# Optimization experiments

Measured on AMD Instinct MI355X. Metric: run time of the kernel, lower is better.

Reference implementation:

```python
import jax, jax.numpy as jnp
import numpy as np

B, T, N, D, FF, E, L, K = 4, 12, 2000, 16, 64, 4, 2, 2
EA, H = 3000, 3
BETA, CW = 0.01, 0.001


def setup_inputs() -> dict:
    key = jax.random.key(0)
    ks = iter(jax.random.split(key, 40))
    nrm = lambda shape, s=0.02: jax.random.normal(next(ks), shape, jnp.float32) * s
    inp = {}
    inp['x'] = jax.random.normal(next(ks), (B, T, N), jnp.float32)
    inp['velo'] = jax.random.uniform(next(ks), (B, T, N), jnp.float32)
    inp['adj_haversine'] = jax.random.uniform(next(ks), (N, N), jnp.float32) + 0.05
    inp['laplacian_diff'] = jax.random.normal(next(ks), (N, N), jnp.float32)
    inp['laplacian_heat'] = jax.random.normal(next(ks), (N, N), jnp.float32)
    inp['start_w'] = nrm((1, D)); inp['start_b'] = jnp.zeros((D,), jnp.float32)
    inp['gate_w'] = nrm((L, D, E))
    inp['exp_w1'] = nrm((L, E, D, FF)); inp['exp_b1'] = jnp.zeros((L, E, FF), jnp.float32)
    inp['exp_w2'] = nrm((L, E, FF, D)); inp['exp_b2'] = jnp.zeros((L, E, D), jnp.float32)
    inp['proj_w'] = nrm((T * D, T)); inp['proj_b'] = jnp.zeros((T,), jnp.float32)
    inp['lt_w'] = nrm((N, EA)); inp['lt_b'] = jnp.zeros((EA,), jnp.float32)
    inp['qkv_w'] = nrm((EA, 3 * EA)); inp['qkv_b'] = jnp.zeros((3 * EA,), jnp.float32)
    inp['attn_out_w'] = nrm((EA, EA)); inp['attn_out_b'] = jnp.zeros((EA,), jnp.float32)
    inp['ll_w'] = nrm((EA, N)); inp['ll_b'] = jnp.zeros((N,), jnp.float32)
    inp['p2_w'] = nrm((T, T)); inp['p2_b'] = jnp.zeros((T,), jnp.float32)
    return inp


def reference(x, velo, adj_haversine, laplacian_diff, laplacian_heat, start_w, start_b,
              gate_w, exp_w1, exp_b1, exp_w2, exp_b2, proj_w, proj_b, lt_w, lt_b,
              qkv_w, qkv_b, attn_out_w, attn_out_b, ll_w, ll_b, p2_w, p2_b):
    # start_fc: [B,T,N,1] -> [B,T,N,D]
    out = x[..., None] @ start_w + start_b
    balance = jnp.float32(0.0)
    cv = lambda v: v.var() / (v.mean() ** 2 + 1e-10)
    for l in range(L):  # AMS mixture-of-experts stack (noisy top-k gating, eval mode)
        feat = out.mean(axis=(1, 2))                      # [B,D]
        logits = feat @ gate_w[l]                          # [B,E]
        topv, topi = jax.lax.top_k(logits, K)
        g = jax.nn.softmax(topv, axis=-1)
        gates = jnp.zeros((B, E), out.dtype).at[jnp.arange(B)[:, None], topi].set(g)
        h = jax.nn.gelu(jnp.einsum('btnd,edf->ebtnf', out, exp_w1[l]) + exp_b1[l][:, None, None, None, :])
        y = jnp.einsum('ebtnf,efd->ebtnd', h, exp_w2[l]) + exp_b2[l][:, None, None, None, :]
        out = out + jnp.einsum('be,ebtnd->btnd', gates, y)  # residual_connection
        imp = gates.sum(0)
        load = (gates > 0).astype(out.dtype).sum(0)
        balance = balance + cv(imp) + cv(load)
    # wavelet layer: 1-level smoothing split along time
    low = lambda z: 0.5 * (z + jnp.roll(z, 1, axis=1))
    low_T = low(x)
    high_V = velo - low(velo)
    # navier-stokes-style graph laplacian from velocities
    v0 = velo[0, 0]                                        # [N]
    G = jnp.maximum(0.0, v0[:, None] / adj_haversine)
    G = jnp.where(jnp.isinf(G), 0.0, G)
    lap_ns = jnp.diag(G.sum(1)) - G
    std = lambda m: (m - m.mean()) / m.std()
    lap_d = std(laplacian_diff); lap_h = std(laplacian_heat)
    lap_ns = jnp.nan_to_num(std(lap_ns))
    # trunk projection: [B,T,N,D] -> [B,T,N]
    outp = (out.transpose(0, 2, 1, 3).reshape(B, N, T * D) @ proj_w + proj_b).transpose(0, 2, 1)
    # laplacian-fused matmuls
    r1 = low_T @ lap_d; r2 = high_V @ lap_ns; r3 = low_T @ lap_h
    rng01 = lambda m: (m - m.min()) / jnp.maximum(m.max() - m.min(), 1e-8)
    lin = lambda m: (rng01(m) @ lt_w + lt_b).transpose(1, 0, 2)   # [T,B,EA]
    r1, r2, r3 = lin(r1), lin(r2), lin(r3)
    hd = EA // H
    wq, wk, wv = jnp.split(qkv_w, 3, axis=1)
    bq, bk, bv = jnp.split(qkv_b, 3)
    def mha(q, k, v):
        qh = (q @ wq + bq).reshape(T, B, H, hd)
        kh = (k @ wk + bk).reshape(T, B, H, hd)
        vh = (v @ wv + bv).reshape(T, B, H, hd)
        sc = jnp.einsum('sbhd,tbhd->bhst', qh, kh) * (1.0 / np.sqrt(hd))
        a = jax.nn.softmax(sc, axis=-1)
        o = jnp.einsum('bhst,tbhd->sbhd', a, vh).reshape(T, B, EA)
        return o @ attn_out_w + attn_out_b
    o1 = mha(r1, r2, r3); o2 = mha(r2, r3, r1); o3 = mha(r3, r1, r2)
    back = lambda o: (o @ ll_w + ll_b).transpose(1, 0, 2)         # [B,T,N]
    out2 = BETA * (back(o1) + back(o2) + back(o3))
    out2 = (out2.reshape(-1, T) @ p2_w + p2_b).reshape(B, N, T).transpose(0, 2, 1)
    out_3 = outp + out2
    # contrastive loss between trunk and laplacian branch
    f1 = outp.transpose(0, 2, 1).reshape(B * N, T)
    f2 = out2.transpose(0, 2, 1).reshape(B * N, T)
    nz = lambda f: f / jnp.maximum(jnp.linalg.norm(f, axis=1, keepdims=True), 1e-12)
    sim = (nz(f1) @ nz(f2).T) / 0.1                               # [8000, 8000]
    closs = -jnp.mean(jnp.diagonal(jax.nn.log_softmax(sim, axis=1)))
    return out_3, balance, CW * closs
```

## Files before the change

kernel.cpp:

```cpp
#include <hip/hip_runtime.h>
#include <math.h>

namespace {
constexpr int B_ = 4, T_ = 12, N_ = 2000, D_ = 16, FF_ = 64, E_ = 4, L_ = 2;
constexpr int EA_ = 3000, H_ = 3, HD_ = EA_ / H_;
constexpr int BT_ = B_ * T_;
constexpr int R3_ = 3 * BT_;
constexpr long long NN_ = (long long)N_ * N_;
constexpr int BTN_ = B_ * T_ * N_;
constexpr float BETA_ = 0.01f, CW_ = 0.001f;
constexpr int RKS_ = 20;
constexpr int RKC_ = 100;
constexpr int KP3 = 3008;
constexpr int KP2 = 2016;

constexpr size_t OFF_OUT4 = 0;
constexpr size_t OFF_LOWT = OFF_OUT4 + (size_t)BTN_ * D_;
constexpr size_t OFF_HVT  = OFF_LOWT + BTN_;
constexpr size_t OFF_ALIN = OFF_HVT + BTN_;
constexpr size_t OFF_RT   = OFF_ALIN + (size_t)N_ * R3_;
constexpr size_t OFF_P    = OFF_RT + (size_t)EA_ * R3_;
constexpr size_t OFF_AOT  = OFF_P + (size_t)R3_ * 3 * EA_;
constexpr size_t OFF_OT   = OFF_AOT + (size_t)EA_ * R3_;
constexpr size_t OFF_O2P  = OFF_OT + (size_t)EA_ * R3_;
constexpr size_t OFF_OUTP = OFF_O2P + BTN_;
constexpr size_t OFF_O2F  = OFF_OUTP + BTN_;
constexpr size_t OFF_LI   = OFF_O2F + BTN_;
constexpr size_t OFF_S    = OFF_LI + 8000;
constexpr size_t OFF_RSL  = OFF_S + 2000;
constexpr size_t OFF_RSH  = OFF_RSL + 48;
constexpr size_t OFF_STP  = OFF_RSH + 48;
constexpr size_t OFF_STAT = OFF_STP + 3072;
constexpr size_t OFF_MMP  = OFF_STAT + 8;
constexpr size_t OFF_AB   = OFF_MMP + 384;
constexpr size_t OFF_CSP  = OFF_AB + 8;
constexpr size_t OFF_CS   = OFF_CSP + 48000;
constexpr size_t OFF_FEAT = OFF_CS + 3000;
constexpr size_t OFF_GATE = OFF_FEAT + 64;
constexpr size_t OFF_BAL  = OFF_GATE + 16;
constexpr size_t OFF_PART = ((OFF_BAL + 1 + 255) & ~(size_t)255);
constexpr size_t PARTCAP  = 13000000;
constexpr size_t OFF_AT_LIN= OFF_PART + PARTCAP;
constexpr size_t OFF_AT_Q  = OFF_AT_LIN + (size_t)R3_ * KP2 / 2;
constexpr size_t OFF_AT_AO = OFF_AT_Q + (size_t)R3_ * KP3 / 2;
constexpr size_t OFF_AT_LL = OFF_AT_AO + (size_t)R3_ * KP3 / 2;
constexpr size_t OFF_G1B   = OFF_AT_LL + (size_t)R3_ * KP3 / 2;
constexpr size_t OFF_G2B   = OFF_G1B + 128000;
}

typedef __attribute__((ext_vector_type(8))) short short8;
typedef __attribute__((ext_vector_type(4))) float f32x4;

__device__ __forceinline__ float waveReduceSum(float v) {
  for (int off = 32; off; off >>= 1) v += __shfl_down(v, off);
  return v;
}

__device__ __forceinline__ unsigned short f2bf(float x) {
  unsigned int u = __float_as_uint(x);
  unsigned int r = (u + 0x7FFFu + ((u >> 16) & 1u)) >> 16;
  return (unsigned short)r;
}

__device__ __forceinline__ size_t aidx(int row, int k) {
  return ((size_t)(k >> 3) * R3_ + row) * 8 + (k & 7);
}

__device__ __forceinline__ void fma16(float* __restrict__ acc,
                                      const float4* __restrict__ a4, float bv) {
#pragma unroll
  for (int r4 = 0; r4 < 4; ++r4) {
    float4 av = a4[r4];
    acc[r4 * 4 + 0] = fmaf(av.x, bv, acc[r4 * 4 + 0]);
    acc[r4 * 4 + 1] = fmaf(av.y, bv, acc[r4 * 4 + 1]);
    acc[r4 * 4 + 2] = fmaf(av.z, bv, acc[r4 * 4 + 2]);
    acc[r4 * 4 + 3] = fmaf(av.w, bv, acc[r4 * 4 + 3]);
  }
}

__global__ void k_init(float* ws) {
  if (threadIdx.x == 0) ws[OFF_BAL] = 0.f;
}

__global__ void k_start(const float* __restrict__ x, const float* __restrict__ sw,
                        const float* __restrict__ sb, float* __restrict__ out4) {
  int i = blockIdx.x * 256 + threadIdx.x;
  if (i >= BTN_ * D_) return;
  int d = i & 15;
  out4[i] = fmaf(x[i >> 4], sw[d], sb[d]);
}

__global__ void k_feat(const float* __restrict__ out4, float* __restrict__ feat) {
  int b = blockIdx.x >> 4, d = blockIdx.x & 15;
  float s = 0.f;
  for (int tn = threadIdx.x; tn < T_ * N_; tn += 256)
    s += out4[((size_t)b * T_ * N_ + tn) * D_ + d];
  __shared__ float red[4];
  s = waveReduceSum(s);
  if ((threadIdx.x & 63) == 0) red[threadIdx.x >> 6] = s;
  __syncthreads();
  if (threadIdx.x == 0)
    feat[blockIdx.x] = (red[0] + red[1] + red[2] + red[3]) * (1.f / (T_ * N_));
}

__global__ void k_gate(const float* __restrict__ feat, const float* __restrict__ gw,
                       float* __restrict__ ws, int l) {
  __shared__ float lg[B_ * E_];
  int tid = threadIdx.x;
  if (tid < B_ * E_) {
    int b = tid >> 2, e = tid & 3;
    float s = 0.f;
    for (int d = 0; d < D_; ++d) s = fmaf(feat[b * D_ + d], gw[(l * D_ + d) * E_ + e], s);
    lg[tid] = s;
  }
  __syncthreads();
  if (tid == 0) {
    float* gates = ws + OFF_GATE;
    float imp[E_] = {0, 0, 0, 0}, load[E_] = {0, 0, 0, 0};
    for (int i = 0; i < B_ * E_; ++i) gates[i] = 0.f;
    for (int b = 0; b < B_; ++b) {
      const float* lb = lg + b * E_;
      int i1 = 0; float v1 = lb[0];
      for (int e = 1; e < E_; ++e) if (lb[e] > v1) { v1 = lb[e]; i1 = e; }
      int i2 = -1; float v2 = -1e30f;
      for (int e = 0; e < E_; ++e) { if (e == i1) continue; if (lb[e] > v2) { v2 = lb[e]; i2 = e; } }
      float e2 = expf(v2 - v1);
      float den = 1.f + e2;
      float g1 = 1.f / den, g2 = e2 / den;
      gates[b * E_ + i1] = g1; gates[b * E_ + i2] = g2;
      imp[i1] += g1; imp[i2] += g2; load[i1] += 1.f; load[i2] += 1.f;
    }
    float bal = 0.f;
    float m = 0.f; for (int e = 0; e < E_; ++e) m += imp[e]; m *= 0.25f;
    float v = 0.f; for (int e = 0; e < E_; ++e) { float d = imp[e] - m; v += d * d; } v *= 0.25f;
    bal += v / (m * m + 1e-10f);
    m = 0.f; for (int e = 0; e < E_; ++e) m += load[e]; m *= 0.25f;
    v = 0.f; for (int e = 0; e < E_; ++e) { float d = load[e] - m; v += d * d; } v *= 0.25f;
    bal += v / (m * m + 1e-10f);
    ws[OFF_BAL] += bal;
  }
}

__global__ void k_expert(float* __restrict__ out4, const float* __restrict__ w1,
                         const float* __restrict__ b1, const float* __restrict__ w2,
                         const float* __restrict__ b2, const float* __restrict__ ws, int l) {
  int b = blockIdx.y;
  int tn = blockIdx.x * 256 + threadIdx.x;
  if (tn >= T_ * N_) return;
  float* row = out4 + ((size_t)b * T_ * N_ + tn) * D_;
  float r[D_], acc[D_];
#pragma unroll
  for (int d = 0; d < D_; ++d) { r[d] = row[d]; acc[d] = r[d]; }
  const float* gates = ws + OFF_GATE;
  for (int e = 0; e < E_; ++e) {
    float g = gates[b * E_ + e];
    if (g <= 0.f) continue;
    const float* W1 = w1 + (size_t)(l * E_ + e) * D_ * FF_;
    const float* B1 = b1 + (size_t)(l * E_ + e) * FF_;
    const float* W2 = w2 + (size_t)(l * E_ + e) * FF_ * D_;
    const float* B2 = b2 + (size_t)(l * E_ + e) * D_;
#pragma unroll 4
    for (int f = 0; f < FF_; ++f) {
      float p = B1[f];
#pragma unroll
      for (int d = 0; d < D_; ++d) p = fmaf(r[d], W1[d * FF_ + f], p);
      float c2 = 1.5957691216057308f * (p + 0.044715f * p * p * p);
      float e1 = __expf(-c2);
      float hv = p * __builtin_amdgcn_rcpf(1.f + e1);
      float gh = g * hv;
#pragma unroll
      for (int d = 0; d < D_; ++d) acc[d] = fmaf(gh, W2[f * D_ + d], acc[d]);
    }
#pragma unroll
    for (int d = 0; d < D_; ++d) acc[d] = fmaf(g, B2[d], acc[d]);
  }
#pragma unroll
  for (int d = 0; d < D_; ++d) row[d] = acc[d];
}

__global__ void k_wavelet(const float* __restrict__ x, const float* __restrict__ velo,
                          float* __restrict__ lowT, float* __restrict__ hvT) {
  int i = blockIdx.x * 256 + threadIdx.x;
  if (i >= BTN_) return;
  int b = i / (T_ * N_);
  int t = (i / N_) % T_;
  int n = i % N_;
  int ip = b * T_ * N_ + ((t + T_ - 1) % T_) * N_ + n;
  int row = t * B_ + b;
  lowT[(size_t)n * BT_ + row] = 0.5f * (x[i] + x[ip]);
  hvT[(size_t)n * BT_ + row] = 0.5f * (velo[i] - velo[ip]);
}

__global__ void k_rowsum(const float* __restrict__ lowT, const float* __restrict__ hvT,
                         float* __restrict__ ws) {
  int which = blockIdx.x / BT_;
  int row = blockIdx.x % BT_;
  const float* M = which ? hvT : lowT;
  float s = 0.f;
  for (int n = threadIdx.x; n < N_; n += 256) s += M[(size_t)n * BT_ + row];
  __shared__ float red[4];
  s = waveReduceSum(s);
  if ((threadIdx.x & 63) == 0) red[threadIdx.x >> 6] = s;
  __syncthreads();
  if (threadIdx.x == 0) ws[(which ? OFF_RSH : OFF_RSL) + row] = red[0] + red[1] + red[2] + red[3];
}

__global__ void k_S(const float* __restrict__ adj, const float* __restrict__ v0,
                    float* __restrict__ S) {
  int m = blockIdx.x;
  float vm = v0[m];
  const float* a = adj + (size_t)m * N_;
  float s = 0.f;
  for (int n = threadIdx.x; n < N_; n += 256) s += vm / a[n];
  __shared__ float red[4];
  s = waveReduceSum(s);
  if ((threadIdx.x & 63) == 0) red[threadIdx.x >> 6] = s;
  __syncthreads();
  if (threadIdx.x == 0) S[m] = red[0] + red[1] + red[2] + red[3];
}

__global__ void k_stats3(const float* __restrict__ lapd, const float* __restrict__ laph,
                         const float* __restrict__ adj, const float* __restrict__ v0,
                         const float* __restrict__ S, float* __restrict__ stp) {
  int z = blockIdx.z;
  float s = 0.f, ss = 0.f;
  if (z < 2) {
    const float* M = z ? laph : lapd;
    for (long long i = blockIdx.x * 256 + threadIdx.x; i < NN_; i += 512 * 256) {
      float v = M[i];
      s += v; ss = fmaf(v, v, ss);
    }
  } else {
    for (long long i = blockIdx.x * 256 + threadIdx.x; i < NN_; i += 512 * 256) {
      int m = (int)(i / N_), n = (int)(i % N_);
      float e = -(v0[m] / adj[i]);
      if (m == n) e += S[m];
      s += e; ss = fmaf(e, e, ss);
    }
  }
  __shared__ float r1[4], r2[4];
  for (int off = 32; off; off >>= 1) { s += __shfl_down(s, off); ss += __shfl_down(ss, off); }
  if ((threadIdx.x & 63) == 0) { r1[threadIdx.x >> 6] = s; r2[threadIdx.x >> 6] = ss; }
  __syncthreads();
  if (threadIdx.x == 0) {
    float* p = stp + (size_t)z * 1024;
    p[blockIdx.x * 2] = r1[0] + r1[1] + r1[2] + r1[3];
    p[blockIdx.x * 2 + 1] = r2[0] + r2[1] + r2[2] + r2[3];
  }
}

__global__ void k_stats2(const float* __restrict__ stp, float* __restrict__ stat) {
  int z = blockIdx.x;
  const float* part = stp + (size_t)z * 1024;
  float s = 0.f, ss = 0.f;
  for (int i = threadIdx.x; i < 512; i += 256) { s += part[i * 2]; ss += part[i * 2 + 1]; }
  __shared__ float r1[4], r2[4];
  for (int off = 32; off; off >>= 1) { s += __shfl_down(s, off); ss += __shfl_down(ss, off); }
  if ((threadIdx.x & 63) == 0) { r1[threadIdx.x >> 6] = s; r2[threadIdx.x >> 6] = ss; }
  __syncthreads();
  if (threadIdx.x == 0) {
    float su = r1[0] + r1[1] + r1[2] + r1[3];
    float sq = r2[0] + r2[1] + r2[2] + r2[3];
    float mu = su * (1.f / (float)NN_);
    float var = sq * (1.f / (float)NN_) - mu * mu;
    stat[2 * z] = mu;
    stat[2 * z + 1] = 1.f / sqrtf(var);
  }
}

__global__ __launch_bounds__(256) void k_rgemm3(
    const float* __restrict__ lowT, const float* __restrict__ hvT,
    const float* __restrict__ lapd, const float* __restrict__ laph,
    const float* __restrict__ adj, const float* __restrict__ v0,
    const float* __restrict__ S, float* __restrict__ part) {
  int zz = blockIdx.z;
  int z = zz / 3, rg = zz % 3;
  int col = blockIdx.x * 256 + threadIdx.x;
  int m0 = blockIdx.y * RKC_;
  int m1 = min(N_, m0 + RKC_);
  float acc[16];
#pragma unroll
  for (int r = 0; r < 16; ++r) acc[r] = 0.f;
  if (col < N_) {
    const float* Abase = (z == 1 ? hvT : lowT);
    const float* ap = Abase + (size_t)m0 * BT_ + rg * 16;
    if (z != 1) {
      const float* Bm = z ? laph : lapd;
      const float* bp = Bm + (size_t)m0 * N_ + col;
      int len = m1 - m0;
      int ng = len >> 3;
      float bc[8];
      if (ng > 0) {
#pragma unroll
        for (int u = 0; u < 8; ++u) bc[u] = bp[(size_t)u * N_];
      }
      for (int gi = 0; gi < ng; ++gi) {
        float bn[8];
        bool more = (gi + 1 < ng);
        if (more) {
#pragma unroll
          for (int u = 0; u < 8; ++u) bn[u] = bp[(size_t)(8 + u) * N_];
        }
#pragma unroll
        for (int u = 0; u < 8; ++u)
          fma16(acc, (const float4*)(ap + (size_t)u * BT_), bc[u]);
        ap += (size_t)8 * BT_;
        bp += (size_t)8 * N_;
        if (more) {
#pragma unroll
          for (int u = 0; u < 8; ++u) bc[u] = bn[u];
        }
      }
      for (int m = m0 + (ng << 3); m < m1; ++m) {
        fma16(acc, (const float4*)ap, *bp);
        ap += BT_;
        bp += N_;
      }
    } else {
      const float* jp = adj + (size_t)m0 * N_ + col;
      int len = m1 - m0;
      int ng = len >> 3;
      float jc[8];
      if (ng > 0) {
#pragma unroll
        for (int u = 0; u < 8; ++u) jc[u] = jp[(size_t)u * N_];
      }
      int m = m0;
      for (int gi = 0; gi < ng; ++gi) {
        float jn[8];
        bool more = (gi + 1 < ng);
        if (more) {
#pragma unroll
          for (int u = 0; u < 8; ++u) jn[u] = jp[(size_t)(8 + u) * N_];
        }
#pragma unroll
        for (int u = 0; u < 8; ++u) {
          float bv = -(v0[m + u] / jc[u]);
          if (m + u == col) bv += S[m + u];
          fma16(acc, (const float4*)(ap + (size_t)u * BT_), bv);
        }
        m += 8;
        ap += (size_t)8 * BT_;
        jp += (size_t)8 * N_;
        if (more) {
#pragma unroll
          for (int u = 0; u < 8; ++u) jc[u] = jn[u];
        }
      }
      for (; m < m1; ++m) {
        float bv = -(v0[m] / (*jp));
        if (m == col) bv += S[m];
        fma16(acc, (const float4*)ap, bv);
        ap += BT_;
        jp += N_;
      }
    }
    float* pp = part + (((size_t)z * RKS_ + blockIdx.y) * BT_ + rg * 16) * N_ + col;
#pragma unroll
    for (int r = 0; r < 16; ++r) pp[(size_t)r * N_] = acc[r];
  }
}

__global__ void k_epiR3(const float* __restrict__ part, float* __restrict__ ws,
                        unsigned short* __restrict__ atl) {
  int z = blockIdx.z;
  int n = blockIdx.x * 256 + threadIdx.x;
  int row = blockIdx.y;
  if (n >= KP2) return;
  int arow = z * BT_ + row;
  if (n >= N_) { atl[aidx(arow, n)] = 0; return; }
  const float* base = part + (size_t)z * RKS_ * BT_ * N_;
  float s = 0.f;
  for (int ks = 0; ks < RKS_; ++ks) s += base[((size_t)(ks * BT_ + row)) * N_ + n];
  int statIdx = (z == 0) ? 0 : (z == 1 ? 4 : 2);
  size_t rsOff = (z == 1) ? OFF_RSH : OFF_RSL;
  float mu = ws[OFF_STAT + statIdx], isd = ws[OFF_STAT + statIdx + 1];
  float val = (s - mu * ws[rsOff + row]) * isd;
  ws[OFF_ALIN + (size_t)n * R3_ + arow] = val;
  atl[aidx(arow, n)] = f2bf(val);
}

__global__ __launch_bounds__(256) void k_mfmaW(
    const unsigned short* __restrict__ At, const float* __restrict__ W,
    float* __restrict__ part, int Nc, int Kp, int K, int stepChunk) {
  __shared__ unsigned int lds[2][128][21];
  int tid = threadIdx.x;
  int lane = tid & 63, w = tid >> 6;
  int lr = lane & 15, lo = lane >> 4;
  int colBase = blockIdx.x * 128;
  int stepsTot = Kp / 32;
  int s0 = blockIdx.y * stepChunk;
  int s1 = min(stepsTot, s0 + stepChunk);
  int cg = tid & 31, kr8 = tid >> 5;
  int c0l = 4 * cg;
  bool fullC = (colBase + 128 <= Nc);

  f32x4 acc[18];
#pragma unroll
  for (int mt = 0; mt < 18; ++mt) {
    acc[mt][0] = 0.f; acc[mt][1] = 0.f; acc[mt][2] = 0.f; acc[mt][3] = 0.f;
  }

  auto stage = [&](int s, int buf) {
#pragma unroll
    for (int h = 0; h < 2; ++h) {
      int kp = kr8 + 8 * h;
      int kA = s * 32 + 2 * kp;
      int kB = kA + 1;
      float4 r0 = {0.f, 0.f, 0.f, 0.f}, r1 = {0.f, 0.f, 0.f, 0.f};
      int c0 = colBase + c0l;
      if (fullC) {
        if (kA < K) r0 = *(const float4*)(W + (size_t)kA * Nc + c0);
        if (kB < K) r1 = *(const float4*)(W + (size_t)kB * Nc + c0);
      } else {
        float rr0[4] = {0.f, 0.f, 0.f, 0.f}, rr1[4] = {0.f, 0.f, 0.f, 0.f};
#pragma unroll
        for (int e = 0; e < 4; ++e) {
          if (c0 + e < Nc) {
            if (kA < K) rr0[e] = W[(size_t)kA * Nc + c0 + e];
            if (kB < K) rr1[e] = W[(size_t)kB * Nc + c0 + e];
          }
        }
        r0.x = rr0[0]; r0.y = rr0[1]; r0.z = rr0[2]; r0.w = rr0[3];
        r1.x = rr1[0]; r1.y = rr1[1]; r1.z = rr1[2]; r1.w = rr1[3];
      }
      lds[buf][c0l + 0][kp] = ((unsigned int)f2bf(r1.x) << 16) | f2bf(r0.x);
      lds[buf][c0l + 1][kp] = ((unsigned int)f2bf(r1.y) << 16) | f2bf(r0.y);
      lds[buf][c0l + 2][kp] = ((unsigned int)f2bf(r1.z) << 16) | f2bf(r0.z);
      lds[buf][c0l + 3][kp] = ((unsigned int)f2bf(r1.w) << 16) | f2bf(r0.w);
    }
  };

  if (s0 < s1) stage(s0, 0);
  __syncthreads();

  const unsigned short* ap = At + ((size_t)(s0 * 4 + lo) * R3_ + lr) * 8;
  const size_t apStep = (size_t)4 * R3_ * 8;
  int lcol0 = w * 32 + lr;
  int lcol1 = w * 32 + 16 + lr;
  for (int s = s0; s < s1; ++s) {
    int buf = (s - s0) & 1;
    union { unsigned int u[4]; short8 s8; } b0, b1;
#pragma unroll
    for (int j = 0; j < 4; ++j) {
      b0.u[j] = lds[buf][lcol0][lo * 4 + j];
      b1.u[j] = lds[buf][lcol1][lo * 4 + j];
    }
#pragma unroll
    for (int mt = 0; mt < 9; ++mt) {
      short8 a = *(const short8*)(ap + (size_t)mt * 128);
      acc[mt] = __builtin_amdgcn_mfma_f32_16x16x32_bf16(a, b0.s8, acc[mt], 0, 0, 0);
      acc[9 + mt] = __builtin_amdgcn_mfma_f32_16x16x32_bf16(a, b1.s8, acc[9 + mt], 0, 0, 0);
    }
    if (s + 1 < s1) stage(s + 1, buf ^ 1);
    __syncthreads();
    ap += apStep;
  }

#pragma unroll
  for (int half = 0; half < 2; ++half) {
    int gcol = colBase + w * 32 + half * 16 + lr;
    if (gcol < Nc) {
#pragma unroll
      for (int mt = 0; mt < 9; ++mt) {
        int row = mt * 16 + lo * 4;
        float* pp = part + ((size_t)blockIdx.y * R3_ + row) * Nc + gcol;
        f32x4 a = acc[half * 9 + mt];
        pp[0] = a[0];
        pp[(size_t)Nc] = a[1];
        pp[2 * (size_t)Nc] = a[2];
        pp[3 * (size_t)Nc] = a[3];
      }
    }
  }
}

__global__ void k_minmax(const float* __restrict__ alin, float* __restrict__ mmp) {
  int g = blockIdx.y;
  float mn = 3.4e38f, mx = -3.4e38f;
  for (int i = blockIdx.x * 256 + threadIdx.x; i < N_ * BT_; i += 64 * 256) {
    int n = i / BT_, r = i % BT_;
    float v = alin[(size_t)n * R3_ + g * BT_ + r];
    mn = fminf(mn, v); mx = fmaxf(mx, v);
  }
  __shared__ float rn[4], rx[4];
  for (int off = 32; off; off >>= 1) {
    mn = fminf(mn, __shfl_down(mn, off));
    mx = fmaxf(mx, __shfl_down(mx, off));
  }
  if ((threadIdx.x & 63) == 0) { rn[threadIdx.x >> 6] = mn; rx[threadIdx.x >> 6] = mx; }
  __syncthreads();
  if (threadIdx.x == 0) {
    mn = fminf(fminf(rn[0], rn[1]), fminf(rn[2], rn[3]));
    mx = fmaxf(fmaxf(rx[0], rx[1]), fmaxf(rx[2], rx[3]));
    mmp[(size_t)(g * 64 + blockIdx.x) * 2] = mn;
    mmp[(size_t)(g * 64 + blockIdx.x) * 2 + 1] = mx;
  }
}

__global__ void k_minmax2(float* __restrict__ ws) {
  int g = blockIdx.x;
  int i = threadIdx.x;
  float mn = ws[OFF_MMP + (size_t)(g * 64 + i) * 2];
  float mx = ws[OFF_MMP + (size_t)(g * 64 + i) * 2 + 1];
  for (int off = 32; off; off >>= 1) {
    mn = fminf(mn, __shfl_down(mn, off));
    mx = fmaxf(mx, __shfl_down(mx, off));
  }
  if (i == 0) {
    float denom = fmaxf(mx - mn, 1e-8f);
    float a = 1.f / denom;
    ws[OFF_AB + g * 2] = a;
    ws[OFF_AB + g * 2 + 1] = -mn * a;
  }
}

__global__ void k_colsum(const float* __restrict__ ltw, float* __restrict__ csp) {
  int e = blockIdx.x * 256 + threadIdx.x;
  int ks = blockIdx.y;
  if (e >= EA_) return;
  float s = 0.f;
  for (int n = ks * 125; n < (ks + 1) * 125; ++n) s += ltw[(size_t)n * EA_ + e];
  csp[(size_t)ks * EA_ + e] = s;
}
__global__ void k_colsum2(float* __restrict__ ws) {
  int e = blockIdx.x * 256 + threadIdx.x;
  if (e >= EA_) return;
  float s = 0.f;
  for (int ks = 0; ks < 16; ++ks) s += ws[OFF_CSP + (size_t)ks * EA_ + e];
  ws[OFF_CS + e] = s;
}

__global__ void k_epiLin(const float* __restrict__ part, const float* __restrict__ ltb,
                         float* __restrict__ ws, unsigned short* __restrict__ atq,
                         int ksplit) {
  int e = blockIdx.x * 256 + threadIdx.x;
  int row = blockIdx.y;
  if (e >= KP3) return;
  if (e >= EA_) { atq[aidx(row, e)] = 0; return; }
  float s = 0.f;
  for (int ks = 0; ks < ksplit; ++ks) s += part[((size_t)(ks * R3_ + row)) * EA_ + e];
  int g = row / BT_;
  float a = ws[OFF_AB + g * 2], bb = ws[OFF_AB + g * 2 + 1];
  float val = fmaf(a, s, fmaf(bb, ws[OFF_CS + e], ltb[e]));
  atq[aidx(row, e)] = f2bf(val);
}

__global__ void k_epiQkv(const float* __restrict__ part, const float* __restrict__ qkvb,
                         float* __restrict__ P, int ksplit) {
  int c = blockIdx.x * 256 + threadIdx.x;
  int row = blockIdx.y;
  if (c >= 3 * EA_) return;
  float s = 0.f;
  for (int ks = 0; ks < ksplit; ++ks) s += part[((size_t)(ks * R3_ + row)) * (3 * EA_) + c];
  P[(size_t)row * (3 * EA_) + c] = s + qkvb[c];
}

__global__ void k_attn(const float* __restrict__ P, unsigned short* __restrict__ atao) {
  int mha = blockIdx.y;
  int s_ = blockIdx.x / (B_ * H_);
  int rem = blockIdx.x % (B_ * H_);
  int b = rem / H_, h = rem % H_;
  const int pq[3] = {0, 1, 2}, pk[3] = {1, 2, 0}, pv[3] = {2, 0, 1};
  const float* qrow = P + ((size_t)(pq[mha] * BT_ + s_ * B_ + b)) * (3 * EA_) + h * HD_;
  __shared__ float sc[T_];
  int w = threadIdx.x >> 6, lane = threadIdx.x & 63;
  for (int t = w; t < T_; t += 4) {
    const float* krow = P + ((size_t)(pk[mha] * BT_ + t * B_ + b)) * (3 * EA_) + EA_ + h * HD_;
    float p = 0.f;
    for (int d = lane; d < HD_; d += 64) p = fmaf(qrow[d], krow[d], p);
    p = waveReduceSum(p);
    if (lane == 0) sc[t] = p * 0.031622776601683794f;
  }
  __syncthreads();
  float a[T_];
  float m = sc[0];
#pragma unroll
  for (int t = 1; t < T_; ++t) m = fmaxf(m, sc[t]);
  float sum = 0.f;
#pragma unroll
  for (int t = 0; t < T_; ++t) { a[t] = expf(sc[t] - m); sum += a[t]; }
  float inv = 1.f / sum;
#pragma unroll
  for (int t = 0; t < T_; ++t) a[t] *= inv;
  int orow = mha * BT_ + s_ * B_ + b;
  for (int d = threadIdx.x; d < HD_; d += 256) {
    float o = 0.f;
#pragma unroll
    for (int t = 0; t < T_; ++t)
      o = fmaf(a[t], P[((size_t)(pv[mha] * BT_ + t * B_ + b)) * (3 * EA_) + 2 * EA_ + h * HD_ + d], o);
    atao[aidx(orow, h * HD_ + d)] = f2bf(o);
  }
  if (h == 0 && threadIdx.x < 8) atao[aidx(orow, EA_ + threadIdx.x)] = 0;
}

__global__ void k_epiAO(const float* __restrict__ part, const float* __restrict__ aob,
                        unsigned short* __restrict__ atll, int ksplit) {
  int c = blockIdx.x * 256 + threadIdx.x;
  int row = blockIdx.y;
  if (c >= KP3) return;
  if (c >= EA_) { atll[aidx(row, c)] = 0; return; }
  float s = 0.f;
  for (int ks = 0; ks < ksplit; ++ks) s += part[((size_t)(ks * R3_ + row)) * EA_ + c];
  atll[aidx(row, c)] = f2bf(s + aob[c]);
}

__global__ void k_epiLL(const float* __restrict__ part, const float* __restrict__ llb,
                        float* __restrict__ o2p, int ksplit) {
  int n = blockIdx.x * 256 + threadIdx.x;
  int row = blockIdx.y;
  if (n >= N_) return;
  float s = 0.f;
  for (int g = 0; g < 3; ++g)
    for (int ks = 0; ks < ksplit; ++ks)
      s += part[((size_t)(ks * R3_ + g * BT_ + row)) * N_ + n];
  int t = row / B_, b = row % B_;
  o2p[(size_t)b * (T_ * N_) + t * N_ + n] = BETA_ * (s + 3.f * llb[n]);
}

__global__ void k_proj(const float* __restrict__ out4, const float* __restrict__ pw,
                       const float* __restrict__ pb, float* __restrict__ outp) {
  int i = blockIdx.x * 256 + threadIdx.x;
  if (i >= BTN_) return;
  int b = i / (T_ * N_);
  int t = (i / N_) % T_;
  int n = i % N_;
  float acc = pb[t];
  for (int t2 = 0; t2 < T_; ++t2) {
    const float* o = out4 + ((size_t)(b * T_ + t2) * N_ + n) * D_;
#pragma unroll
    for (int d = 0; d < D_; ++d) acc = fmaf(o[d], pw[(t2 * D_ + d) * T_ + t], acc);
  }
  outp[i] = acc;
}

__global__ void k_p2(const float* __restrict__ o2p, const float* __restrict__ p2w,
                     const float* __restrict__ p2b, float* __restrict__ o2f) {
  int i = blockIdx.x * 256 + threadIdx.x;
  if (i >= BTN_) return;
  int b = i / (T_ * N_);
  int t = (i / N_) % T_;
  int n = i % N_;
  float acc = p2b[t];
  const float* src = o2p + (size_t)b * (T_ * N_) + (size_t)n * T_;
#pragma unroll
  for (int c = 0; c < T_; ++c) acc = fmaf(src[c], p2w[c * T_ + t], acc);
  o2f[i] = acc;
}

__global__ void k_fng(const float* __restrict__ outp, const float* __restrict__ o2f,
                      float* __restrict__ dout, unsigned short* __restrict__ g1b,
                      unsigned short* __restrict__ g2b) {
  int r = blockIdx.x * 256 + threadIdx.x;
  if (r >= B_ * N_) return;
  int b = r / N_, n = r % N_;
  float v1[T_], v2[T_];
  float s1 = 0.f, s2 = 0.f;
#pragma unroll
  for (int t = 0; t < T_; ++t) {
    size_t idx = (size_t)b * T_ * N_ + (size_t)t * N_ + n;
    v1[t] = outp[idx];
    v2[t] = o2f[idx];
    dout[idx] = v1[t] + v2[t];
    s1 = fmaf(v1[t], v1[t], s1);
    s2 = fmaf(v2[t], v2[t], s2);
  }
  float n1 = fmaxf(sqrtf(s1), 1e-12f), n2 = fmaxf(sqrtf(s2), 1e-12f);
  float i1 = 10.f / n1, i2 = 1.f / n2;
  unsigned short q[32], z[32];
#pragma unroll
  for (int t = 0; t < T_; ++t) { q[t] = f2bf(v1[t] * i1); z[t] = f2bf(v2[t] * i2); }
#pragma unroll
  for (int t = T_; t < 32; ++t) { q[t] = 0; z[t] = 0; }
  short8* qd = (short8*)(g1b + (size_t)r * 32);
  short8* zd = (short8*)(g2b + (size_t)r * 32);
#pragma unroll
  for (int c = 0; c < 4; ++c) {
    short8 pv, pz;
#pragma unroll
    for (int e = 0; e < 8; ++e) { pv[e] = (short)q[c * 8 + e]; pz[e] = (short)z[c * 8 + e]; }
    qd[c] = pv;
    zd[c] = pz;
  }
}

__global__ __launch_bounds__(256) void k_lsemf(const unsigned short* __restrict__ g1b,
                                               const unsigned short* __restrict__ g2b,
                                               float* __restrict__ psm,
                                               float* __restrict__ psd) {
  int lane = threadIdx.x & 63, w = threadIdx.x >> 6;
  int lr = lane & 15, lo = lane >> 4;
  int i0 = blockIdx.x * 16;
  int slice = blockIdx.y * 4 + w;
  short8 a = *(const short8*)(g1b + (size_t)(i0 + lr) * 32 + lo * 8);
  float sm[4] = {0.f, 0.f, 0.f, 0.f};
  float sd[4] = {0.f, 0.f, 0.f, 0.f};
  for (int t = slice; t < 500; t += 16) {
    int j0 = t * 16;
    short8 b = *(const short8*)(g2b + (size_t)(j0 + lr) * 32 + lo * 8);
    f32x4 acc = {0.f, 0.f, 0.f, 0.f};
    acc = __builtin_amdgcn_mfma_f32_16x16x32_bf16(a, b, acc, 0, 0, 0);
#pragma unroll
    for (int rg = 0; rg < 4; ++rg) {
      float s = acc[rg];
      sm[rg] += __expf(s);
      if (j0 + lr == i0 + lo * 4 + rg) sd[rg] = s;
    }
  }
#pragma unroll
  for (int off = 1; off < 16; off <<= 1) {
#pragma unroll
    for (int rg = 0; rg < 4; ++rg) {
      sm[rg] += __shfl_xor(sm[rg], off);
      sd[rg] += __shfl_xor(sd[rg], off);
    }
  }
  __shared__ float lsm[4][16], lsd[4][16];
  if (lr == 0) {
#pragma unroll
    for (int rg = 0; rg < 4; ++rg) {
      lsm[w][lo * 4 + rg] = sm[rg];
      lsd[w][lo * 4 + rg] = sd[rg];
    }
  }
  __syncthreads();
  if (threadIdx.x < 16) {
    float m = lsm[0][threadIdx.x] + lsm[1][threadIdx.x] + lsm[2][threadIdx.x] + lsm[3][threadIdx.x];
    float d = lsd[0][threadIdx.x] + lsd[1][threadIdx.x] + lsd[2][threadIdx.x] + lsd[3][threadIdx.x];
    psm[(size_t)blockIdx.y * 8000 + i0 + threadIdx.x] = m;
    psd[(size_t)blockIdx.y * 8000 + i0 + threadIdx.x] = d;
  }
}

__global__ __launch_bounds__(1024) void k_lsefin(const float* __restrict__ psm,
                                                 const float* __restrict__ psd,
                                                 const float* __restrict__ ws,
                                                 float* __restrict__ dout) {
  float acc = 0.f;
  for (int r = threadIdx.x; r < B_ * N_; r += 1024) {
    float sm = psm[r] + psm[8000 + r] + psm[16000 + r] + psm[24000 + r];
    float sd = psd[r] + psd[8000 + r] + psd[16000 + r] + psd[24000 + r];
    acc += sd - logf(sm);
  }
  __shared__ float red[16];
  acc = waveReduceSum(acc);
  if ((threadIdx.x & 63) == 0) red[threadIdx.x >> 6] = acc;
  __syncthreads();
  if (threadIdx.x == 0) {
    float s = 0.f;
    for (int i = 0; i < 16; ++i) s += red[i];
    float closs = -s * (1.f / (B_ * N_));
    dout[BTN_] = ws[OFF_BAL];
    dout[BTN_ + 1] = CW_ * closs;
  }
}

extern "C" void kernel_launch(void* const* d_in, const int* in_sizes, int n_in,
                              void* d_out, int out_size, void* d_ws, size_t ws_size,
                              hipStream_t stream) {
  const float* x    = (const float*)d_in[0];
  const float* velo = (const float*)d_in[1];
  const float* adj  = (const float*)d_in[2];
  const float* lapd = (const float*)d_in[3];
  const float* laph = (const float*)d_in[4];
  const float* sw   = (const float*)d_in[5];
  const float* sb   = (const float*)d_in[6];
  const float* gw   = (const float*)d_in[7];
  const float* ew1  = (const float*)d_in[8];
  const float* eb1  = (const float*)d_in[9];
  const float* ew2  = (const float*)d_in[10];
  const float* eb2  = (const float*)d_in[11];
  const float* pw   = (const float*)d_in[12];
  const float* pb   = (const float*)d_in[13];
  const float* ltw  = (const float*)d_in[14];
  const float* ltb  = (const float*)d_in[15];
  const float* qkvw = (const float*)d_in[16];
  const float* qkvb = (const float*)d_in[17];
  const float* aow  = (const float*)d_in[18];
  const float* aob  = (const float*)d_in[19];
  const float* llw  = (const float*)d_in[20];
  const float* llb  = (const float*)d_in[21];
  const float* p2w  = (const float*)d_in[22];
  const float* p2b  = (const float*)d_in[23];
  float* ws = (float*)d_ws;
  float* dout = (float*)d_out;
  const float* v0 = velo;
  float* part = ws + OFF_PART;
  unsigned short* atLin = (unsigned short*)(ws + OFF_AT_LIN);
  unsigned short* atQ   = (unsigned short*)(ws + OFF_AT_Q);
  unsigned short* atAO  = (unsigned short*)(ws + OFF_AT_AO);
  unsigned short* atLL  = (unsigned short*)(ws + OFF_AT_LL);
  unsigned short* g1b   = (unsigned short*)(ws + OFF_G1B);
  unsigned short* g2b   = (unsigned short*)(ws + OFF_G2B);
  dim3 b256(256);

  k_init<<<dim3(1), dim3(64), 0, stream>>>(ws);

  k_start<<<dim3((BTN_ * D_ + 255) / 256), b256, 0, stream>>>(x, sw, sb, ws + OFF_OUT4);

  for (int l = 0; l < L_; ++l) {
    k_feat<<<dim3(B_ * D_), b256, 0, stream>>>(ws + OFF_OUT4, ws + OFF_FEAT);
    k_gate<<<dim3(1), dim3(64), 0, stream>>>(ws + OFF_FEAT, gw, ws, l);
    k_expert<<<dim3((T_ * N_ + 255) / 256, B_), b256, 0, stream>>>(ws + OFF_OUT4, ew1, eb1, ew2, eb2, ws, l);
  }

  k_wavelet<<<dim3((BTN_ + 255) / 256), b256, 0, stream>>>(x, velo, ws + OFF_LOWT, ws + OFF_HVT);
  k_rowsum<<<dim3(2 * BT_), b256, 0, stream>>>(ws + OFF_LOWT, ws + OFF_HVT, ws);
  k_S<<<dim3(N_), b256, 0, stream>>>(adj, v0, ws + OFF_S);

  k_stats3<<<dim3(512, 1, 3), b256, 0, stream>>>(lapd, laph, adj, v0, ws + OFF_S, ws + OFF_STP);
  k_stats2<<<dim3(3), b256, 0, stream>>>(ws + OFF_STP, ws + OFF_STAT);

  k_rgemm3<<<dim3(8, RKS_, 9), b256, 0, stream>>>(ws + OFF_LOWT, ws + OFF_HVT, lapd, laph,
                                                  adj, v0, ws + OFF_S, part);
  k_epiR3<<<dim3(8, 48, 3), b256, 0, stream>>>(part, ws, atLin);

  k_minmax<<<dim3(64, 3), b256, 0, stream>>>(ws + OFF_ALIN, ws + OFF_MMP);
  k_minmax2<<<dim3(3), dim3(64), 0, stream>>>(ws);
  k_colsum<<<dim3(12, 16), b256, 0, stream>>>(ltw, ws + OFF_CSP);
  k_colsum2<<<dim3(12), b256, 0, stream>>>(ws);

  k_mfmaW<<<dim3(24, 21), b256, 0, stream>>>(atLin, ltw, part, EA_, KP2, N_, 3);
  k_epiLin<<<dim3(12, 144), b256, 0, stream>>>(part, ltb, ws, atQ, 21);

  k_mfmaW<<<dim3(71, 10), b256, 0, stream>>>(atQ, qkvw, part, 3 * EA_, KP3, EA_, 10);
  k_epiQkv<<<dim3(36, 144), b256, 0, stream>>>(part, qkvb, ws + OFF_P, 10);

  k_attn<<<dim3(T_ * B_ * H_, 3), b256, 0, stream>>>(ws + OFF_P, atAO);

  k_mfmaW<<<dim3(24, 24), b256, 0, stream>>>(atAO, aow, part, EA_, KP3, EA_, 4);
  k_epiAO<<<dim3(12, 144), b256, 0, stream>>>(part, aob, atLL, 24);

  k_mfmaW<<<dim3(16, 24), b256, 0, stream>>>(atLL, llw, part, N_, KP3, EA_, 4);
  k_epiLL<<<dim3(8, 48), b256, 0, stream>>>(part, llb, ws + OFF_O2P, 24);

  k_proj<<<dim3((BTN_ + 255) / 256), b256, 0, stream>>>(ws + OFF_OUT4, pw, pb, ws + OFF_OUTP);
  k_p2<<<dim3((BTN_ + 255) / 256), b256, 0, stream>>>(ws + OFF_O2P, p2w, p2b, ws + OFF_O2F);

  k_fng<<<dim3((B_ * N_ + 255) / 256), b256, 0, stream>>>(ws + OFF_OUTP, ws + OFF_O2F, dout, g1b, g2b);

  k_lsemf<<<dim3(500, 4), b256, 0, stream>>>(g1b, g2b, part, part + 32000);
  k_lsefin<<<dim3(1), dim3(1024), 0, stream>>>(part, part + 32000, ws, dout);
}
```

Before: 524.0 us.

## Fuse matrix mean/variance stats into rgemm3 and retune split-K counts

Removes the separate k_stats3 pass, which reread three 2000x2000 matrices (lapd, laph, and the adj-derived matrix), and instead accumulates sum and sum-of-squares inside k_rgemm3 while those matrices are already being streamed. Only blocks with rg==0 accumulate, and k_stats2 now reduces 160 partials instead of 512. It also changes the split-K chunk counts of several k_mfmaW GEMMs and their epilogues. The stats work adds a small amount of arithmetic to the GEMM inner loop, and stats2 must now run after rgemm3.

```diff
diff --git a/kernel.cpp b/kernel.cpp
--- a/kernel.cpp
+++ b/kernel.cpp
@@ -219,41 +219,11 @@
   if (threadIdx.x == 0) S[m] = red[0] + red[1] + red[2] + red[3];
 }
 
-__global__ void k_stats3(const float* __restrict__ lapd, const float* __restrict__ laph,
-                         const float* __restrict__ adj, const float* __restrict__ v0,
-                         const float* __restrict__ S, float* __restrict__ stp) {
-  int z = blockIdx.z;
-  float s = 0.f, ss = 0.f;
-  if (z < 2) {
-    const float* M = z ? laph : lapd;
-    for (long long i = blockIdx.x * 256 + threadIdx.x; i < NN_; i += 512 * 256) {
-      float v = M[i];
-      s += v; ss = fmaf(v, v, ss);
-    }
-  } else {
-    for (long long i = blockIdx.x * 256 + threadIdx.x; i < NN_; i += 512 * 256) {
-      int m = (int)(i / N_), n = (int)(i % N_);
-      float e = -(v0[m] / adj[i]);
-      if (m == n) e += S[m];
-      s += e; ss = fmaf(e, e, ss);
-    }
-  }
-  __shared__ float r1[4], r2[4];
-  for (int off = 32; off; off >>= 1) { s += __shfl_down(s, off); ss += __shfl_down(ss, off); }
-  if ((threadIdx.x & 63) == 0) { r1[threadIdx.x >> 6] = s; r2[threadIdx.x >> 6] = ss; }
-  __syncthreads();
-  if (threadIdx.x == 0) {
-    float* p = stp + (size_t)z * 1024;
-    p[blockIdx.x * 2] = r1[0] + r1[1] + r1[2] + r1[3];
-    p[blockIdx.x * 2 + 1] = r2[0] + r2[1] + r2[2] + r2[3];
-  }
-}
-
 __global__ void k_stats2(const float* __restrict__ stp, float* __restrict__ stat) {
   int z = blockIdx.x;
   const float* part = stp + (size_t)z * 1024;
   float s = 0.f, ss = 0.f;
-  for (int i = threadIdx.x; i < 512; i += 256) { s += part[i * 2]; ss += part[i * 2 + 1]; }
+  for (int i = threadIdx.x; i < 160; i += 256) { s += part[i * 2]; ss += part[i * 2 + 1]; }
   __shared__ float r1[4], r2[4];
   for (int off = 32; off; off >>= 1) { s += __shfl_down(s, off); ss += __shfl_down(ss, off); }
   if ((threadIdx.x & 63) == 0) { r1[threadIdx.x >> 6] = s; r2[threadIdx.x >> 6] = ss; }
@@ -272,12 +242,15 @@
     const float* __restrict__ lowT, const float* __restrict__ hvT,
     const float* __restrict__ lapd, const float* __restrict__ laph,
     const float* __restrict__ adj, const float* __restrict__ v0,
-    const float* __restrict__ S, float* __restrict__ part) {
+    const float* __restrict__ S, float* __restrict__ part,
+    float* __restrict__ stp) {
   int zz = blockIdx.z;
   int z = zz / 3, rg = zz % 3;
   int col = blockIdx.x * 256 + threadIdx.x;
   int m0 = blockIdx.y * RKC_;
   int m1 = min(N_, m0 + RKC_);
+  bool doStats = (rg == 0);
+  float sAcc = 0.f, ssAcc = 0.f;
   float acc[16];
 #pragma unroll
   for (int r = 0; r < 16; ++r) acc[r] = 0.f;
@@ -302,8 +275,10 @@
           for (int u = 0; u < 8; ++u) bn[u] = bp[(size_t)(8 + u) * N_];
         }
 #pragma unroll
-        for (int u = 0; u < 8; ++u)
+        for (int u = 0; u < 8; ++u) {
           fma16(acc, (const float4*)(ap + (size_t)u * BT_), bc[u]);
+          if (doStats) { sAcc += bc[u]; ssAcc = fmaf(bc[u], bc[u], ssAcc); }
+        }
         ap += (size_t)8 * BT_;
         bp += (size_t)8 * N_;
         if (more) {
@@ -312,7 +287,9 @@
         }
       }
       for (int m = m0 + (ng << 3); m < m1; ++m) {
-        fma16(acc, (const float4*)ap, *bp);
+        float bv = *bp;
+        fma16(acc, (const float4*)ap, bv);
+        if (doStats) { sAcc += bv; ssAcc = fmaf(bv, bv, ssAcc); }
         ap += BT_;
         bp += N_;
       }
@@ -338,6 +315,7 @@
           float bv = -(v0[m + u] / jc[u]);
           if (m + u == col) bv += S[m + u];
           fma16(acc, (const float4*)(ap + (size_t)u * BT_), bv);
+          if (doStats) { sAcc += bv; ssAcc = fmaf(bv, bv, ssAcc); }
         }
         m += 8;
         ap += (size_t)8 * BT_;
@@ -351,6 +329,7 @@
         float bv = -(v0[m] / (*jp));
         if (m == col) bv += S[m];
         fma16(acc, (const float4*)ap, bv);
+        if (doStats) { sAcc += bv; ssAcc = fmaf(bv, bv, ssAcc); }
         ap += BT_;
         jp += N_;
       }
@@ -358,6 +337,18 @@
     float* pp = part + (((size_t)z * RKS_ + blockIdx.y) * BT_ + rg * 16) * N_ + col;
 #pragma unroll
     for (int r = 0; r < 16; ++r) pp[(size_t)r * N_] = acc[r];
+  }
+  if (doStats) {
+    __shared__ float r1[4], r2[4];
+    float s = sAcc, ss = ssAcc;
+    for (int off = 32; off; off >>= 1) { s += __shfl_down(s, off); ss += __shfl_down(ss, off); }
+    if ((threadIdx.x & 63) == 0) { r1[threadIdx.x >> 6] = s; r2[threadIdx.x >> 6] = ss; }
+    __syncthreads();
+    if (threadIdx.x == 0) {
+      float* p = stp + (size_t)z * 1024 + ((size_t)blockIdx.y * 8 + blockIdx.x) * 2;
+      p[0] = r1[0] + r1[1] + r1[2] + r1[3];
+      p[1] = r2[0] + r2[1] + r2[2] + r2[3];
+    }
   }
 }
 
@@ -808,11 +799,9 @@
   k_rowsum<<<dim3(2 * BT_), b256, 0, stream>>>(ws + OFF_LOWT, ws + OFF_HVT, ws);
   k_S<<<dim3(N_), b256, 0, stream>>>(adj, v0, ws + OFF_S);
 
-  k_stats3<<<dim3(512, 1, 3), b256, 0, stream>>>(lapd, laph, adj, v0, ws + OFF_S, ws + OFF_STP);
+  k_rgemm3<<<dim3(8, RKS_, 9), b256, 0, stream>>>(ws + OFF_LOWT, ws + OFF_HVT, lapd, laph,
+                                                  adj, v0, ws + OFF_S, part, ws + OFF_STP);
   k_stats2<<<dim3(3), b256, 0, stream>>>(ws + OFF_STP, ws + OFF_STAT);
-
-  k_rgemm3<<<dim3(8, RKS_, 9), b256, 0, stream>>>(ws + OFF_LOWT, ws + OFF_HVT, lapd, laph,
-                                                  adj, v0, ws + OFF_S, part);
   k_epiR3<<<dim3(8, 48, 3), b256, 0, stream>>>(part, ws, atLin);
 
   k_minmax<<<dim3(64, 3), b256, 0, stream>>>(ws + OFF_ALIN, ws + OFF_MMP);
@@ -820,19 +809,19 @@
   k_colsum<<<dim3(12, 16), b256, 0, stream>>>(ltw, ws + OFF_CSP);
   k_colsum2<<<dim3(12), b256, 0, stream>>>(ws);
 
-  k_mfmaW<<<dim3(24, 21), b256, 0, stream>>>(atLin, ltw, part, EA_, KP2, N_, 3);
-  k_epiLin<<<dim3(12, 144), b256, 0, stream>>>(part, ltb, ws, atQ, 21);
+  k_mfmaW<<<dim3(24, 16), b256, 0, stream>>>(atLin, ltw, part, EA_, KP2, N_, 4);
+  k_epiLin<<<dim3(12, 144), b256, 0, stream>>>(part, ltb, ws, atQ, 16);
 
   k_mfmaW<<<dim3(71, 10), b256, 0, stream>>>(atQ, qkvw, part, 3 * EA_, KP3, EA_, 10);
   k_epiQkv<<<dim3(36, 144), b256, 0, stream>>>(part, qkvb, ws + OFF_P, 10);
 
   k_attn<<<dim3(T_ * B_ * H_, 3), b256, 0, stream>>>(ws + OFF_P, atAO);
 
-  k_mfmaW<<<dim3(24, 24), b256, 0, stream>>>(atAO, aow, part, EA_, KP3, EA_, 4);
-  k_epiAO<<<dim3(12, 144), b256, 0, stream>>>(part, aob, atLL, 24);
-
-  k_mfmaW<<<dim3(16, 24), b256, 0, stream>>>(atLL, llw, part, N_, KP3, EA_, 4);
-  k_epiLL<<<dim3(8, 48), b256, 0, stream>>>(part, llb, ws + OFF_O2P, 24);
+  k_mfmaW<<<dim3(24, 16), b256, 0, stream>>>(atAO, aow, part, EA_, KP3, EA_, 6);
+  k_epiAO<<<dim3(12, 144), b256, 0, stream>>>(part, aob, atLL, 16);
+
+  k_mfmaW<<<dim3(16, 20), b256, 0, stream>>>(atLL, llw, part, N_, KP3, EA_, 5);
+  k_epiLL<<<dim3(8, 48), b256, 0, stream>>>(part, llb, ws + OFF_O2P, 20);
 
   k_proj<<<dim3((BTN_ + 255) / 256), b256, 0, stream>>>(ws + OFF_OUT4, pw, pb, ws + OFF_OUTP);
   k_p2<<<dim3((BTN_ + 255) / 256), b256, 0, stream>>>(ws + OFF_O2P, p2w, p2b, ws + OFF_O2F);
```

After: 501.1 us. 4.4% less time.
